# Optimization experiments

Measured on AMD Instinct MI355X. Metric: run time of the kernel, lower is better.

## Reference

```python
import jax, jax.numpy as jnp
import numpy as np

NALPHABET = 128
NEMBEDDING = 128
NSTATE = 512


def setup_inputs() -> dict:
    key = jax.random.key(0)
    k_w, k_emb, k_win, k_bin, k_wout, k_bout = jax.random.split(key, 6)
    b, t = 256, 256
    w = jax.random.randint(k_w, (b, t), 0, NALPHABET, dtype=jnp.int64)
    emb = jax.random.normal(k_emb, (NALPHABET, NEMBEDDING), dtype=jnp.float32)
    fan_in = NEMBEDDING + NSTATE
    bound_in = 1.0 / np.sqrt(fan_in)
    W_in = jax.random.uniform(k_win, (NSTATE, fan_in), jnp.float32, -bound_in, bound_in)
    b_in = jax.random.uniform(k_bin, (NSTATE,), jnp.float32, -bound_in, bound_in)
    bound_out = 1.0 / np.sqrt(NSTATE)
    W_out = jax.random.uniform(k_wout, (NALPHABET, NSTATE), jnp.float32, -bound_out, bound_out)
    b_out = jax.random.uniform(k_bout, (NALPHABET,), jnp.float32, -bound_out, bound_out)
    return {"w": w, "emb": emb, "W_in": W_in, "b_in": b_in, "W_out": W_out, "b_out": b_out}


def reference(w, emb, W_in, b_in, W_out, b_out):
    b = w.shape[0]
    nstate = W_in.shape[0]
    f = emb[w]  # (b, t, nembedding)
    # Split W_in into embedding and state blocks: cat((f_t, state)) @ W_in.T
    W_f = W_in[:, : emb.shape[1]]  # (nstate, nembedding)
    W_s = W_in[:, emb.shape[1]:]   # (nstate, nstate)
    # Precompute input contributions for all timesteps at once.
    fin = jnp.einsum("bte,ne->btn", f, W_f) + b_in  # (b, t, nstate)

    def step(state, fin_t):
        state_next = jnp.tanh(fin_t + state @ W_s.T)
        return state_next, state_next

    state0 = jnp.zeros((b, nstate), dtype=jnp.float32)
    _, states = jax.lax.scan(step, state0, jnp.swapaxes(fin, 0, 1))
    states = jnp.swapaxes(states, 0, 1)  # (b, t, nstate)
    y = jnp.einsum("btn,an->bta", states, W_out) + b_out  # (b, t, nalphabet)
    return y
```

## Files before the change

kernel.cpp:

```cpp
#include <hip/hip_runtime.h>
#include <stdint.h>
#include <math.h>

#define NALPH 128
#define NEMB  128
#define NST   512
#define BATCH 256
#define TLEN  256
#define FANIN 640

#define SDOT4(a, b, c) __builtin_amdgcn_sdot4((a), (b), (c), false)
typedef __attribute__((ext_vector_type(4))) int i32x4;

#define BAR_LDS() do {                                            \
    asm volatile("s_waitcnt lgkmcnt(0)\n\ts_barrier" ::: "memory"); \
    __builtin_amdgcn_sched_barrier(0);                            \
  } while (0)

__global__ __launch_bounds__(256) void k_prep(
    const float* __restrict__ emb, const float* __restrict__ W_in,
    const float* __restrict__ b_in, const float* __restrict__ W_out,
    float* __restrict__ G, int* __restrict__ WqT, float* __restrict__ Sd,
    int* __restrict__ WoQ, int* __restrict__ WoF, float* __restrict__ So,
    int* __restrict__ WsF)
{
  int bid = blockIdx.x, tid = threadIdx.x;
  if (bid < 256) {
    int idx = bid * 256 + tid;
    int tok = idx >> 9, n = idx & 511;
    const float4* er = (const float4*)(emb + tok * NEMB);
    const float4* wr = (const float4*)(W_in + (size_t)n * FANIN);
    float acc = b_in[n];
#pragma unroll 8
    for (int e4 = 0; e4 < NEMB / 4; ++e4) {
      float4 a = er[e4];
      float4 b = wr[e4];
      acc = fmaf(a.x, b.x, acc);
      acc = fmaf(a.y, b.y, acc);
      acc = fmaf(a.z, b.z, acc);
      acc = fmaf(a.w, b.w, acc);
    }
    G[idx] = acc;
  } else if (bid < 768) {
    int n = bid - 256;
    __shared__ float smax[128];
    float lw[4]; float m = 0.f;
    if (tid < 128) {
      float4 v = *(const float4*)(W_in + (size_t)n * FANIN + NEMB + tid * 4);
      lw[0] = v.x; lw[1] = v.y; lw[2] = v.z; lw[3] = v.w;
#pragma unroll
      for (int i = 0; i < 4; ++i) m = fmaxf(m, fabsf(lw[i]));
      smax[tid] = m;
    }
    __syncthreads();
    for (int s2 = 64; s2 > 0; s2 >>= 1) {
      if (tid < s2) smax[tid] = fmaxf(smax[tid], smax[tid + s2]);
      __syncthreads();
    }
    float mx = smax[0];
    if (tid < 128) {
      float r = 127.f / mx;
      uint32_t pk = 0;
#pragma unroll
      for (int i = 0; i < 4; ++i) {
        int qv = (int)rintf(lw[i] * r);
        qv = qv < -127 ? -127 : (qv > 127 ? 127 : qv);
        pk |= (uint32_t)(qv & 0xff) << (8 * i);
      }
      WqT[tid * NST + n] = (int)pk;
      int kd = tid;
      int c = kd >> 4, hi = (kd >> 2) & 3, d = kd & 3;
      int lane = hi * 16 + (n & 15), nt = n >> 4;
      WsF[(((nt * 8 + c) * 64) + lane) * 4 + d] = (int)pk;
    }
    if (tid == 0) Sd[n] = mx / 16129.0f;
  } else {
    int a = bid - 768;
    __shared__ float smax[128];
    float lw[4]; float m = 0.f;
    if (tid < 128) {
      float4 v = *(const float4*)(W_out + (size_t)a * NST + tid * 4);
      lw[0] = v.x; lw[1] = v.y; lw[2] = v.z; lw[3] = v.w;
#pragma unroll
      for (int i = 0; i < 4; ++i) m = fmaxf(m, fabsf(lw[i]));
      smax[tid] = m;
    }
    __syncthreads();
    for (int s2 = 64; s2 > 0; s2 >>= 1) {
      if (tid < s2) smax[tid] = fmaxf(smax[tid], smax[tid + s2]);
      __syncthreads();
    }
    float mx = smax[0];
    if (tid < 128) {
      float r = 127.f / mx;
      uint32_t pk = 0;
#pragma unroll
      for (int i = 0; i < 4; ++i) {
        int qv = (int)rintf(lw[i] * r);
        qv = qv < -127 ? -127 : (qv > 127 ? 127 : qv);
        pk |= (uint32_t)(qv & 0xff) << (8 * i);
      }
      WoQ[tid * 128 + a] = (int)pk;
      int kd = tid;
      int c = kd >> 4, hi = (kd >> 2) & 3, d = kd & 3;
      int lane = hi * 16 + (a & 15), ta = a >> 4;
      WoF[(((ta * 8 + c) * 64) + lane) * 4 + d] = (int)pk;
    }
    if (tid == 0) So[a] = mx / 16129.0f;
  }
}

__global__ __launch_bounds__(512, 1) void k_rec(
    const int* __restrict__ w, const float* __restrict__ G,
    const int* __restrict__ WsF, const float* __restrict__ Sd,
    signed char* __restrict__ qstates)
{
  __shared__ __align__(16) signed char qs[2][NST];
  int tid  = threadIdx.x;
  int lane = tid & 63, wv = tid >> 6;
  int l15  = lane & 15, hi = lane >> 4;
  int row  = blockIdx.x;

  const i32x4* wsf = (const i32x4*)WsF;
  i32x4 Bf[4][8];
#pragma unroll
  for (int q = 0; q < 4; ++q)
#pragma unroll
    for (int c = 0; c < 8; ++c)
      Bf[q][c] = wsf[((size_t)((wv * 4 + q) * 8 + c)) * 64 + lane];

  float dn = Sd[tid];
  const int* wr = w + row * TLEN;
  float g = G[wr[0] * NST + tid];

  qs[0][tid] = 0;
  __syncthreads();

  signed char* qrow = qstates + (size_t)row * TLEN * NST + tid;

  int p = 0;
  for (int t = 0; t < TLEN; ++t) {
    int tok_n = (t < TLEN - 1) ? wr[t + 1] : 0;
    float g_n = G[tok_n * NST + tid];

    i32x4 A[8];
#pragma unroll
    for (int c = 0; c < 8; ++c)
      A[c] = *(const i32x4*)(qs[p] + c * 64 + hi * 16);

    i32x4 acc0 = {0,0,0,0}, acc1 = {0,0,0,0}, acc2 = {0,0,0,0}, acc3 = {0,0,0,0};
#pragma unroll
    for (int c = 0; c < 8; ++c) {
      acc0 = __builtin_amdgcn_mfma_i32_16x16x64_i8(A[c], Bf[0][c], acc0, 0, 0, 0);
      acc1 = __builtin_amdgcn_mfma_i32_16x16x64_i8(A[c], Bf[1][c], acc1, 0, 0, 0);
      acc2 = __builtin_amdgcn_mfma_i32_16x16x64_i8(A[c], Bf[2][c], acc2, 0, 0, 0);
      acc3 = __builtin_amdgcn_mfma_i32_16x16x64_i8(A[c], Bf[3][c], acc3, 0, 0, 0);
    }

    int vm = (hi & 1) ? ((hi & 2) ? acc3[0] : acc1[0])
                      : ((hi & 2) ? acc2[0] : acc0[0]);

    float a = g + (float)vm * dn;
    a = fminf(fmaxf(a, -15.f), 15.f);
    float e = __expf(2.f * a);
    float s = fmaf(-2.f, __builtin_amdgcn_rcpf(e + 1.f), 1.f);
    signed char q8 = (signed char)(int)rintf(s * 127.f);
    qs[p ^ 1][tid] = q8;
    qrow[(size_t)t * NST] = q8;
    BAR_LDS();
    g = g_n;
    p ^= 1;
  }
}

__global__ __launch_bounds__(256) void k_out_mfma(
    const signed char* __restrict__ qstates, const int* __restrict__ WoF,
    const float* __restrict__ So, const float* __restrict__ b_out,
    float* __restrict__ y)
{
  int tid = threadIdx.x;
  int lane = tid & 63, wv = tid >> 6;
  int l15 = lane & 15, hi = lane >> 4;
  size_t bt0 = (size_t)blockIdx.x * 64 + (size_t)wv * 16;

  const signed char* abase = qstates + (bt0 + l15) * NST + hi * 16;
  i32x4 A[8];
#pragma unroll
  for (int c = 0; c < 8; ++c) A[c] = *(const i32x4*)(abase + c * 64);

  const i32x4* wf = (const i32x4*)WoF;
#pragma unroll
  for (int ta = 0; ta < 8; ++ta) {
    const i32x4* bbase = wf + (size_t)ta * 8 * 64 + lane;
    i32x4 acc = {0, 0, 0, 0};
#pragma unroll
    for (int c = 0; c < 8; ++c)
      acc = __builtin_amdgcn_mfma_i32_16x16x64_i8(A[c], bbase[c * 64], acc, 0, 0, 0);
    int a = ta * 16 + l15;
    float s = So[a], b = b_out[a];
    float* yb = y + (bt0 + hi * 4) * 128 + a;
#pragma unroll
    for (int r = 0; r < 4; ++r) yb[(size_t)r * 128] = (float)acc[r] * s + b;
  }
}

__global__ __launch_bounds__(256) void k_out_i8(
    const signed char* __restrict__ qstates, const int* __restrict__ WoQ,
    const float* __restrict__ So, const float* __restrict__ b_out,
    float* __restrict__ y)
{
  __shared__ __align__(16) int sl[32 * 128];
  int tid = threadIdx.x;
  size_t bt0 = (size_t)blockIdx.x * 32;
  const int4* gp = (const int4*)(qstates + bt0 * NST);
  int4* slp = (int4*)sl;
#pragma unroll
  for (int i = 0; i < 4; ++i) slp[tid + 256 * i] = gp[tid + 256 * i];
  __syncthreads();

  int a0 = tid & 63, gidx = tid >> 6;
  const int* slg = sl + gidx * 8 * 128;
  int acc0[8], acc1[8];
#pragma unroll
  for (int r = 0; r < 8; ++r) { acc0[r] = 0; acc1[r] = 0; }

  for (int j4 = 0; j4 < 32; ++j4) {
    int w00 = WoQ[(4 * j4 + 0) * 128 + a0];
    int w01 = WoQ[(4 * j4 + 0) * 128 + a0 + 64];
    int w10 = WoQ[(4 * j4 + 1) * 128 + a0];
    int w11 = WoQ[(4 * j4 + 1) * 128 + a0 + 64];
    int w20 = WoQ[(4 * j4 + 2) * 128 + a0];
    int w21 = WoQ[(4 * j4 + 2) * 128 + a0 + 64];
    int w30 = WoQ[(4 * j4 + 3) * 128 + a0];
    int w31 = WoQ[(4 * j4 + 3) * 128 + a0 + 64];
#pragma unroll
    for (int r = 0; r < 8; ++r) {
      int4 s = *(const int4*)&slg[r * 128 + 4 * j4];
      acc0[r] = SDOT4(w00, s.x, acc0[r]);
      acc1[r] = SDOT4(w01, s.x, acc1[r]);
      acc0[r] = SDOT4(w10, s.y, acc0[r]);
      acc1[r] = SDOT4(w11, s.y, acc1[r]);
      acc0[r] = SDOT4(w20, s.z, acc0[r]);
      acc1[r] = SDOT4(w21, s.z, acc1[r]);
      acc0[r] = SDOT4(w30, s.w, acc0[r]);
      acc1[r] = SDOT4(w31, s.w, acc1[r]);
    }
  }

  float s0 = So[a0], s1 = So[a0 + 64];
  float b0 = b_out[a0], b1 = b_out[a0 + 64];
#pragma unroll
  for (int r = 0; r < 8; ++r) {
    size_t rowb = (bt0 + gidx * 8 + r) * 128;
    y[rowb + a0]      = (float)acc0[r] * s0 + b0;
    y[rowb + a0 + 64] = (float)acc1[r] * s1 + b1;
  }
}

extern "C" void kernel_launch(void* const* d_in, const int* in_sizes, int n_in,
                              void* d_out, int out_size, void* d_ws, size_t ws_size,
                              hipStream_t stream) {
  const int*   w     = (const int*)d_in[0];
  const float* emb   = (const float*)d_in[1];
  const float* W_in  = (const float*)d_in[2];
  const float* b_in  = (const float*)d_in[3];
  const float* W_out = (const float*)d_in[4];
  const float* b_out = (const float*)d_in[5];
  float* y = (float*)d_out;

  char* ws = (char*)d_ws;
  float*       G       = (float*)ws;
  int*         WqT     = (int*)(ws + (256 << 10));
  float*       Sd      = (float*)(ws + (512 << 10));
  int*         WoQ     = (int*)(ws + (576 << 10));
  float*       So      = (float*)(ws + (640 << 10));
  int*         WoF     = (int*)(ws + (704 << 10));
  int*         WsF     = (int*)(ws + (768 << 10));
  signed char* qstates = (signed char*)(ws + (1024 << 10));

  k_prep<<<896, 256, 0, stream>>>(emb, W_in, b_in, W_out, G, WqT, Sd, WoQ, WoF, So, WsF);
  k_rec <<<BATCH, 512, 0, stream>>>(w, G, WsF, Sd, qstates);
  k_out_mfma<<<BATCH * TLEN / 64, 256, 0, stream>>>(qstates, WoF, So, b_out, y);
}
```

Baseline: 266.4 us.

## Transpose embedding weights for coalesced G precompute and stage output through LDS

```diff
diff --git a/kernel.cpp b/kernel.cpp
--- a/kernel.cpp
+++ b/kernel.cpp
@@ -17,30 +17,31 @@
     __builtin_amdgcn_sched_barrier(0);                            \
   } while (0)
 
+__global__ __launch_bounds__(128) void k_tr(
+    const float* __restrict__ W_in, float* __restrict__ WfT)
+{
+  int n = blockIdx.x, e = threadIdx.x;
+  WfT[e * NST + n] = W_in[(size_t)n * FANIN + e];
+}
+
 __global__ __launch_bounds__(256) void k_prep(
     const float* __restrict__ emb, const float* __restrict__ W_in,
     const float* __restrict__ b_in, const float* __restrict__ W_out,
-    float* __restrict__ G, int* __restrict__ WqT, float* __restrict__ Sd,
-    int* __restrict__ WoQ, int* __restrict__ WoF, float* __restrict__ So,
+    const float* __restrict__ WfT,
+    float* __restrict__ G, float* __restrict__ Sd,
+    int* __restrict__ WoF, float* __restrict__ So,
     int* __restrict__ WsF)
 {
   int bid = blockIdx.x, tid = threadIdx.x;
   if (bid < 256) {
-    int idx = bid * 256 + tid;
-    int tok = idx >> 9, n = idx & 511;
-    const float4* er = (const float4*)(emb + tok * NEMB);
-    const float4* wr = (const float4*)(W_in + (size_t)n * FANIN);
+    int tok = bid >> 1;
+    int n   = ((bid & 1) << 8) + tid;
+    const float* eb = emb + tok * NEMB;
     float acc = b_in[n];
 #pragma unroll 8
-    for (int e4 = 0; e4 < NEMB / 4; ++e4) {
-      float4 a = er[e4];
-      float4 b = wr[e4];
-      acc = fmaf(a.x, b.x, acc);
-      acc = fmaf(a.y, b.y, acc);
-      acc = fmaf(a.z, b.z, acc);
-      acc = fmaf(a.w, b.w, acc);
-    }
-    G[idx] = acc;
+    for (int e = 0; e < NEMB; ++e)
+      acc = fmaf(eb[e], WfT[e * NST + n], acc);
+    G[tok * NST + n] = acc;
   } else if (bid < 768) {
     int n = bid - 256;
     __shared__ float smax[128];
@@ -67,7 +68,6 @@
         qv = qv < -127 ? -127 : (qv > 127 ? 127 : qv);
         pk |= (uint32_t)(qv & 0xff) << (8 * i);
       }
-      WqT[tid * NST + n] = (int)pk;
       int kd = tid;
       int c = kd >> 4, hi = (kd >> 2) & 3, d = kd & 3;
       int lane = hi * 16 + (n & 15), nt = n >> 4;
@@ -100,7 +100,6 @@
         qv = qv < -127 ? -127 : (qv > 127 ? 127 : qv);
         pk |= (uint32_t)(qv & 0xff) << (8 * i);
       }
-      WoQ[tid * 128 + a] = (int)pk;
       int kd = tid;
       int c = kd >> 4, hi = (kd >> 2) & 3, d = kd & 3;
       int lane = hi * 16 + (a & 15), ta = a >> 4;
@@ -178,6 +177,7 @@
     const float* __restrict__ So, const float* __restrict__ b_out,
     float* __restrict__ y)
 {
+  __shared__ float sl[64 * 128];
   int tid = threadIdx.x;
   int lane = tid & 63, wv = tid >> 6;
   int l15 = lane & 15, hi = lane >> 4;
@@ -198,63 +198,16 @@
       acc = __builtin_amdgcn_mfma_i32_16x16x64_i8(A[c], bbase[c * 64], acc, 0, 0, 0);
     int a = ta * 16 + l15;
     float s = So[a], b = b_out[a];
-    float* yb = y + (bt0 + hi * 4) * 128 + a;
-#pragma unroll
-    for (int r = 0; r < 4; ++r) yb[(size_t)r * 128] = (float)acc[r] * s + b;
+    float* slb = sl + (wv * 16 + hi * 4) * 128 + a;
+#pragma unroll
+    for (int r = 0; r < 4; ++r) slb[r * 128] = (float)acc[r] * s + b;
   }
-}
-
-__global__ __launch_bounds__(256) void k_out_i8(
-    const signed char* __restrict__ qstates, const int* __restrict__ WoQ,
-    const float* __restrict__ So, const float* __restrict__ b_out,
-    float* __restrict__ y)
-{
-  __shared__ __align__(16) int sl[32 * 128];
-  int tid = threadIdx.x;
-  size_t bt0 = (size_t)blockIdx.x * 32;
-  const int4* gp = (const int4*)(qstates + bt0 * NST);
-  int4* slp = (int4*)sl;
-#pragma unroll
-  for (int i = 0; i < 4; ++i) slp[tid + 256 * i] = gp[tid + 256 * i];
   __syncthreads();
 
-  int a0 = tid & 63, gidx = tid >> 6;
-  const int* slg = sl + gidx * 8 * 128;
-  int acc0[8], acc1[8];
-#pragma unroll
-  for (int r = 0; r < 8; ++r) { acc0[r] = 0; acc1[r] = 0; }
-
-  for (int j4 = 0; j4 < 32; ++j4) {
-    int w00 = WoQ[(4 * j4 + 0) * 128 + a0];
-    int w01 = WoQ[(4 * j4 + 0) * 128 + a0 + 64];
-    int w10 = WoQ[(4 * j4 + 1) * 128 + a0];
-    int w11 = WoQ[(4 * j4 + 1) * 128 + a0 + 64];
-    int w20 = WoQ[(4 * j4 + 2) * 128 + a0];
-    int w21 = WoQ[(4 * j4 + 2) * 128 + a0 + 64];
-    int w30 = WoQ[(4 * j4 + 3) * 128 + a0];
-    int w31 = WoQ[(4 * j4 + 3) * 128 + a0 + 64];
-#pragma unroll
-    for (int r = 0; r < 8; ++r) {
-      int4 s = *(const int4*)&slg[r * 128 + 4 * j4];
-      acc0[r] = SDOT4(w00, s.x, acc0[r]);
-      acc1[r] = SDOT4(w01, s.x, acc1[r]);
-      acc0[r] = SDOT4(w10, s.y, acc0[r]);
-      acc1[r] = SDOT4(w11, s.y, acc1[r]);
-      acc0[r] = SDOT4(w20, s.z, acc0[r]);
-      acc1[r] = SDOT4(w21, s.z, acc1[r]);
-      acc0[r] = SDOT4(w30, s.w, acc0[r]);
-      acc1[r] = SDOT4(w31, s.w, acc1[r]);
-    }
-  }
-
-  float s0 = So[a0], s1 = So[a0 + 64];
-  float b0 = b_out[a0], b1 = b_out[a0 + 64];
-#pragma unroll
-  for (int r = 0; r < 8; ++r) {
-    size_t rowb = (bt0 + gidx * 8 + r) * 128;
-    y[rowb + a0]      = (float)acc0[r] * s0 + b0;
-    y[rowb + a0 + 64] = (float)acc1[r] * s1 + b1;
-  }
+  float4* yb = (float4*)(y + (size_t)blockIdx.x * 64 * 128);
+  const float4* sb = (const float4*)sl;
+#pragma unroll
+  for (int i = 0; i < 8; ++i) yb[i * 256 + tid] = sb[i * 256 + tid];
 }
 
 extern "C" void kernel_launch(void* const* d_in, const int* in_sizes, int n_in,
@@ -270,15 +223,15 @@
 
   char* ws = (char*)d_ws;
   float*       G       = (float*)ws;
-  int*         WqT     = (int*)(ws + (256 << 10));
+  float*       WfT     = (float*)(ws + (256 << 10));
   float*       Sd      = (float*)(ws + (512 << 10));
-  int*         WoQ     = (int*)(ws + (576 << 10));
   float*       So      = (float*)(ws + (640 << 10));
   int*         WoF     = (int*)(ws + (704 << 10));
   int*         WsF     = (int*)(ws + (768 << 10));
   signed char* qstates = (signed char*)(ws + (1024 << 10));
 
-  k_prep<<<896, 256, 0, stream>>>(emb, W_in, b_in, W_out, G, WqT, Sd, WoQ, WoF, So, WsF);
+  k_tr  <<<512, 128, 0, stream>>>(W_in, WfT);
+  k_prep<<<896, 256, 0, stream>>>(emb, W_in, b_in, W_out, WfT, G, Sd, WoF, So, WsF);
   k_rec <<<BATCH, 512, 0, stream>>>(w, G, WsF, Sd, qstates);
   k_out_mfma<<<BATCH * TLEN / 64, 256, 0, stream>>>(qstates, WoF, So, b_out, y);
 }
```

After: 268.5 us. About the same (+0.8%).
